# Kernel tuning notes

Hardware: AMD Instinct MI355X
Metric: run time of the kernel (lower is better)

The kernel has to match this reference:

```python
import jax, jax.numpy as jnp
import numpy as np

N = 262144          # total nodes in batched graph
B = 2048            # number of graphs
IN_DIM = 512        # in_dim == hidden_dim (required by GRUCell usage)
HID = 512
OUT_DIM = 128
TIMESTEPS = 2


def setup_inputs() -> dict:
    key = jax.random.key(0)
    ks = jax.random.split(key, 12)
    s = 0.02
    x = jax.random.normal(ks[0], (N, IN_DIM), dtype=jnp.float32)
    # sorted random segment ids: ragged graph sizes, node -> graph id
    segment_ids = jnp.sort(jax.random.randint(ks[1], (N,), 0, B, dtype=jnp.int32))
    return {
        "x": x,
        "segment_ids": segment_ids,
        "w_att_l": jax.random.normal(ks[2], (IN_DIM,), dtype=jnp.float32) * s,
        "w_att_r": jax.random.normal(ks[3], (IN_DIM,), dtype=jnp.float32) * s,
        "W_node": jax.random.normal(ks[4], (IN_DIM, HID), dtype=jnp.float32) * s,
        "W_ih": jax.random.normal(ks[5], (3 * HID, HID), dtype=jnp.float32) * s,
        "W_hh": jax.random.normal(ks[6], (3 * HID, HID), dtype=jnp.float32) * s,
        "b_ih": jax.random.normal(ks[7], (3 * HID,), dtype=jnp.float32) * s,
        "b_hh": jax.random.normal(ks[8], (3 * HID,), dtype=jnp.float32) * s,
        "W_lin": jax.random.normal(ks[9], (HID, OUT_DIM), dtype=jnp.float32) * s,
        "b_lin": jax.random.normal(ks[10], (OUT_DIM,), dtype=jnp.float32) * s,
    }


def _segment_softmax(alpha, seg, num_segments):
    # numerically stable per-graph softmax over nodes
    m = jax.ops.segment_max(alpha, seg, num_segments=num_segments)
    e = jnp.exp(alpha - m[seg])
    denom = jax.ops.segment_sum(e, seg, num_segments=num_segments)
    return e / denom[seg]


def _gru_cell(inp, h, W_ih, W_hh, b_ih, b_hh):
    gi = inp @ W_ih.T + b_ih          # [B, 3H]
    gh = h @ W_hh.T + b_hh            # [B, 3H]
    gi_r, gi_z, gi_n = jnp.split(gi, 3, axis=-1)
    gh_r, gh_z, gh_n = jnp.split(gh, 3, axis=-1)
    r = jax.nn.sigmoid(gi_r + gh_r)
    z = jax.nn.sigmoid(gi_z + gh_z)
    n = jnp.tanh(gi_n + r * gh_n)
    return (1.0 - z) * n + z * h


def reference(x, segment_ids, w_att_l, w_att_r, W_node, W_ih, W_hh, b_ih, b_hh, W_lin, b_lin):
    seg = segment_ids
    # SumPooling: per-graph sum of node features -> initial GRU hidden state
    out = jax.ops.segment_sum(x, seg, num_segments=B)      # [B, IN_DIM]
    # src_feats (x) are constant across timesteps -> precompute projections
    left_att = x @ w_att_l                                  # [N]
    h_neighbors = x @ W_node                                # [N, HID]
    for _ in range(TIMESTEPS):
        right_att = out @ w_att_r                           # [B]
        alpha = jax.nn.leaky_relu(left_att + right_att[seg], negative_slope=0.01)
        scores = _segment_softmax(alpha, seg, B)            # [N]
        msg = h_neighbors * scores[:, None]                 # [N, HID]
        gat_out = jax.ops.segment_sum(msg, seg, num_segments=B)  # [B, HID]
        h = jax.nn.elu(gat_out)
        # dropout is identity in eval mode
        out = jax.nn.silu(_gru_cell(h, out, W_ih, W_hh, b_ih, b_hh))
    return out @ W_lin + b_lin                              # [B, OUT_DIM]
```

## Files before the change

kernel.cpp:

```cpp
#include <hip/hip_runtime.h>
#include <hip/hip_bf16.h>
#include <cstdint>
#include <cstddef>

#define N_NODES 262144
#define NGRAPH  2048
#define DIM     512
#define HID3    1536
#define OUTD    128

typedef __attribute__((ext_vector_type(8))) short  short8;
typedef __attribute__((ext_vector_type(4))) float  floatx4;
typedef __attribute__((ext_vector_type(2))) float  floatx2;

__device__ inline unsigned short f2bf(float f) {
    union { float f; uint32_t u; } v; v.f = f;
    uint32_t u = v.u;
    return (unsigned short)((u + 0x7fffu + ((u >> 16) & 1u)) >> 16);
}
__device__ inline float bf2f(unsigned short h) {
    union { uint32_t u; float f; } v; v.u = ((uint32_t)h) << 16; return v.f;
}

__device__ __forceinline__ void gload_lds16(const void* g, void* l) {
    __builtin_amdgcn_global_load_lds((const __attribute__((address_space(1))) void*)g,
                                     (__attribute__((address_space(3))) void*)l, 16, 0, 0);
}

__global__ __launch_bounds__(256) void k_prep(const float* __restrict__ Wih,
        const float* __restrict__ Whh, const float* __restrict__ Wnode,
        const int* __restrict__ seg, unsigned short* __restrict__ Wihb,
        unsigned short* __restrict__ Whhb, unsigned short* __restrict__ WnT,
        int* __restrict__ starts) {
    __shared__ float tile[32][33];
    int id = blockIdx.x, t = threadIdx.x;
    if (id < 3072) {
        int i = id * 256 + t; Wihb[i] = f2bf(Wih[i]);
    } else if (id < 6144) {
        int i = (id - 3072) * 256 + t; Whhb[i] = f2bf(Whh[i]);
    } else if (id < 6400) {
        int idx = id - 6144;
        int bx = idx >> 4, by = idx & 15;
        int tx = t & 31, ty = t >> 5;
        for (int r = 0; r < 32; r += 8)
            tile[ty + r][tx] = Wnode[(size_t)(bx * 32 + ty + r) * DIM + by * 32 + tx];
        __syncthreads();
        for (int r = 0; r < 32; r += 8)
            WnT[(size_t)(by * 32 + ty + r) * DIM + bx * 32 + tx] = f2bf(tile[tx][ty + r]);
    } else {
        int b = (id - 6400) * 256 + t;
        if (b <= NGRAPH) {
            int lo = 0, hi = N_NODES;
            while (lo < hi) { int mid = (lo + hi) >> 1; if (seg[mid] < b) lo = mid + 1; else hi = mid; }
            starts[b] = lo;
        }
    }
}

template<bool WRITE_XQ>
__global__ __launch_bounds__(256) void k_init(const float* __restrict__ x,
        const int* __restrict__ starts, const float* __restrict__ watl,
        float* __restrict__ left_att, float* __restrict__ hcur,
        unsigned short* __restrict__ hcur_bf, unsigned char* __restrict__ xq) {
    __shared__ float wl[DIM];
    __shared__ float red[4 * DIM];
    int b = blockIdx.x, t = threadIdx.x;
    wl[t] = watl[t]; wl[t + 256] = watl[t + 256];
    __syncthreads();
    int s = starts[b], e = starts[b + 1];
    int w = t >> 6, lane = t & 63;
    int f0 = lane * 4;
    float acc[8] = {0.f,0.f,0.f,0.f,0.f,0.f,0.f,0.f};

    auto proc = [&](int i, floatx4 v0, floatx4 v1) {
        acc[0] += v0[0]; acc[1] += v0[1]; acc[2] += v0[2]; acc[3] += v0[3];
        acc[4] += v1[0]; acc[5] += v1[1]; acc[6] += v1[2]; acc[7] += v1[3];
        float dot = v0[0]*wl[f0] + v0[1]*wl[f0+1] + v0[2]*wl[f0+2] + v0[3]*wl[f0+3]
                  + v1[0]*wl[256+f0] + v1[1]*wl[256+f0+1] + v1[2]*wl[256+f0+2] + v1[3]*wl[256+f0+3];
        #pragma unroll
        for (int off = 32; off > 0; off >>= 1) dot += __shfl_xor(dot, off);
        if (lane == 0) left_att[i] = dot;
        if constexpr (WRITE_XQ) {
            unsigned int q0 = (unsigned int)__builtin_amdgcn_cvt_pk_fp8_f32(v0[0], v0[1], 0, false);
            q0 = (unsigned int)__builtin_amdgcn_cvt_pk_fp8_f32(v0[2], v0[3], (int)q0, true);
            unsigned int q1 = (unsigned int)__builtin_amdgcn_cvt_pk_fp8_f32(v1[0], v1[1], 0, false);
            q1 = (unsigned int)__builtin_amdgcn_cvt_pk_fp8_f32(v1[2], v1[3], (int)q1, true);
            *reinterpret_cast<unsigned int*>(xq + (size_t)i * DIM + f0) = q0;
            *reinterpret_cast<unsigned int*>(xq + (size_t)i * DIM + 256 + f0) = q1;
        }
    };

    int i = s + w;
    for (; i + 4 < e; i += 8) {
        floatx4 a0 = __builtin_nontemporal_load(reinterpret_cast<const floatx4*>(x + (size_t)i * DIM + f0));
        floatx4 a1 = __builtin_nontemporal_load(reinterpret_cast<const floatx4*>(x + (size_t)i * DIM + 256 + f0));
        floatx4 b0 = __builtin_nontemporal_load(reinterpret_cast<const floatx4*>(x + (size_t)(i + 4) * DIM + f0));
        floatx4 b1 = __builtin_nontemporal_load(reinterpret_cast<const floatx4*>(x + (size_t)(i + 4) * DIM + 256 + f0));
        proc(i, a0, a1);
        proc(i + 4, b0, b1);
    }
    if (i < e) {
        floatx4 a0 = __builtin_nontemporal_load(reinterpret_cast<const floatx4*>(x + (size_t)i * DIM + f0));
        floatx4 a1 = __builtin_nontemporal_load(reinterpret_cast<const floatx4*>(x + (size_t)i * DIM + 256 + f0));
        proc(i, a0, a1);
    }

    #pragma unroll
    for (int j = 0; j < 4; j++) {
        red[w * DIM + f0 + j]       = acc[j];
        red[w * DIM + 256 + f0 + j] = acc[4 + j];
    }
    __syncthreads();
    float s0 = red[t]       + red[DIM + t]       + red[2*DIM + t]       + red[3*DIM + t];
    float s1 = red[256 + t] + red[DIM + 256 + t] + red[2*DIM + 256 + t] + red[3*DIM + 256 + t];
    hcur[(size_t)b * DIM + t] = s0;
    hcur[(size_t)b * DIM + 256 + t] = s1;
    hcur_bf[(size_t)b * DIM + t] = f2bf(s0);
    hcur_bf[(size_t)b * DIM + 256 + t] = f2bf(s1);
}

template<bool XQ>
__global__ __launch_bounds__(256) void k_att(const float* __restrict__ x,
        const unsigned char* __restrict__ xq, const float* __restrict__ left,
        const int* __restrict__ starts, const float* __restrict__ hcur,
        const float* __restrict__ watr, unsigned short* __restrict__ swbf) {
    __shared__ float red[4 * DIM];
    __shared__ float rsh[4];
    __shared__ float rsm[4];
    __shared__ float rscal[4];
    int b = blockIdx.x, t = threadIdx.x;
    int w = t >> 6, lane = t & 63;

    float p = hcur[(size_t)b * DIM + t] * watr[t] + hcur[(size_t)b * DIM + 256 + t] * watr[256 + t];
    #pragma unroll
    for (int off = 32; off > 0; off >>= 1) p += __shfl_xor(p, off);
    if (lane == 0) rsh[w] = p;
    int s = starts[b], e = starts[b + 1];
    __syncthreads();
    float ra = rsh[0] + rsh[1] + rsh[2] + rsh[3];

    float m = -1e30f;
    for (int i = s + t; i < e; i += 256) {
        float a = left[i] + ra; a = a >= 0.f ? a : 0.01f * a;
        m = fmaxf(m, a);
    }
    #pragma unroll
    for (int off = 32; off > 0; off >>= 1) m = fmaxf(m, __shfl_xor(m, off));
    if (lane == 0) rsm[w] = m;
    __syncthreads();
    m = fmaxf(fmaxf(rsm[0], rsm[1]), fmaxf(rsm[2], rsm[3]));

    float acc[8] = {0.f,0.f,0.f,0.f,0.f,0.f,0.f,0.f};
    float esum = 0.f;
    if constexpr (XQ) {
        int f0 = lane * 8;
        auto qacc = [&](uint2 q, float ev) {
            floatx2 p0 = __builtin_amdgcn_cvt_pk_f32_fp8((int)q.x, false);
            floatx2 p1 = __builtin_amdgcn_cvt_pk_f32_fp8((int)q.x, true);
            floatx2 p2 = __builtin_amdgcn_cvt_pk_f32_fp8((int)q.y, false);
            floatx2 p3 = __builtin_amdgcn_cvt_pk_f32_fp8((int)q.y, true);
            acc[0] += ev * p0[0]; acc[1] += ev * p0[1];
            acc[2] += ev * p1[0]; acc[3] += ev * p1[1];
            acc[4] += ev * p2[0]; acc[5] += ev * p2[1];
            acc[6] += ev * p3[0]; acc[7] += ev * p3[1];
        };
        int i = s + w;
        for (; i + 4 < e; i += 8) {
            uint2 q0 = *reinterpret_cast<const uint2*>(xq + (size_t)i * DIM + f0);
            uint2 q1 = *reinterpret_cast<const uint2*>(xq + (size_t)(i + 4) * DIM + f0);
            float a0 = left[i] + ra;     a0 = a0 >= 0.f ? a0 : 0.01f * a0;
            float a1 = left[i + 4] + ra; a1 = a1 >= 0.f ? a1 : 0.01f * a1;
            float e0 = __expf(a0 - m), e1 = __expf(a1 - m);
            esum += e0 + e1;
            qacc(q0, e0);
            qacc(q1, e1);
        }
        if (i < e) {
            uint2 q0 = *reinterpret_cast<const uint2*>(xq + (size_t)i * DIM + f0);
            float a0 = left[i] + ra; a0 = a0 >= 0.f ? a0 : 0.01f * a0;
            float e0 = __expf(a0 - m);
            esum += e0;
            qacc(q0, e0);
        }
        #pragma unroll
        for (int j = 0; j < 8; j++) red[w * DIM + f0 + j] = acc[j];
    } else {
        int f0 = lane * 4;
        for (int i = s + w; i < e; i += 4) {
            float a0 = left[i] + ra; a0 = a0 >= 0.f ? a0 : 0.01f * a0;
            float e0 = __expf(a0 - m);
            esum += e0;
            float4 v0 = *reinterpret_cast<const float4*>(x + (size_t)i * DIM + f0);
            float4 v1 = *reinterpret_cast<const float4*>(x + (size_t)i * DIM + 256 + f0);
            acc[0] += e0 * v0.x; acc[1] += e0 * v0.y; acc[2] += e0 * v0.z; acc[3] += e0 * v0.w;
            acc[4] += e0 * v1.x; acc[5] += e0 * v1.y; acc[6] += e0 * v1.z; acc[7] += e0 * v1.w;
        }
        #pragma unroll
        for (int j = 0; j < 4; j++) {
            red[w * DIM + f0 + j]       = acc[j];
            red[w * DIM + 256 + f0 + j] = acc[4 + j];
        }
    }
    #pragma unroll
    for (int off = 32; off > 0; off >>= 1) esum += __shfl_xor(esum, off);
    if (lane == 0) rscal[w] = esum;
    __syncthreads();
    float tot = rscal[0] + rscal[1] + rscal[2] + rscal[3];
    float inv = tot > 0.f ? 1.0f / tot : 0.0f;
    float s0 = (red[t]       + red[DIM + t]       + red[2*DIM + t]       + red[3*DIM + t])       * inv;
    float s1 = (red[256 + t] + red[DIM + 256 + t] + red[2*DIM + 256 + t] + red[3*DIM + 256 + t]) * inv;
    swbf[(size_t)b * DIM + t] = f2bf(s0);
    swbf[(size_t)b * DIM + 256 + t] = f2bf(s1);
}

__global__ __launch_bounds__(256, 2) void k_gemm(const unsigned short* __restrict__ A0,
        const unsigned short* __restrict__ Wt0, float* __restrict__ Cf0,
        unsigned short* __restrict__ Cb0, int Ncols0, int ny0,
        const unsigned short* __restrict__ A1, const unsigned short* __restrict__ Wt1,
        float* __restrict__ Cf1, unsigned short* __restrict__ Cb1, int Ncols1) {
    const int z = blockIdx.z;
    if (z == 0 && (int)blockIdx.y >= ny0) return;
    const unsigned short* A  = z ? A1  : A0;
    const unsigned short* Wt = z ? Wt1 : Wt0;
    float* Cf          = z ? Cf1 : Cf0;
    unsigned short* Cb = z ? Cb1 : Cb0;
    const int Ncols    = z ? Ncols1 : Ncols0;

    __shared__ __align__(16) unsigned short lA[2][128 * 64];
    __shared__ __align__(16) unsigned short lW[2][128 * 64];

    int t = threadIdx.x;
    int w = t >> 6, lane = t & 63;
    int wr = w >> 1, wc = w & 1;
    int mbase = blockIdx.x * 128;
    int nbase = blockIdx.y * 128;
    int fr = lane & 15, hi = lane >> 4;
    int swz_r = (fr & 7) << 4;

    int rbase = t >> 3;
    int cole = ((((t & 7) * 16) ^ ((rbase & 7) << 4)) >> 1);
    int ldsoff = t * 16;

    floatx4 acc[4][4];
    #pragma unroll
    for (int m = 0; m < 4; m++)
        #pragma unroll
        for (int n = 0; n < 4; n++) {
            acc[m][n][0] = 0.f; acc[m][n][1] = 0.f; acc[m][n][2] = 0.f; acc[m][n][3] = 0.f;
        }

    const unsigned short* gA = A  + (size_t)(mbase + rbase) * DIM + cole;
    const unsigned short* gW = Wt + (size_t)(nbase + rbase) * DIM + cole;

    auto stage = [&](int kk, int buf) {
        #pragma unroll
        for (int c = 0; c < 4; ++c) {
            gload_lds16(gA + (size_t)(c * 32) * DIM + kk, (char*)&lA[buf][0] + c * 4096 + ldsoff);
            gload_lds16(gW + (size_t)(c * 32) * DIM + kk, (char*)&lW[buf][0] + c * 4096 + ldsoff);
        }
    };

    stage(0, 0);
    __syncthreads();
    int cur = 0;
    for (int it = 0; it < 8; ++it) {
        if (it < 7) stage((it + 1) * 64, cur ^ 1);
        #pragma unroll
        for (int ks = 0; ks < 2; ++ks) {
            short8 af[4], bf[4];
            int bc = (ks * 64 + hi * 16) ^ swz_r;
            #pragma unroll
            for (int m = 0; m < 4; ++m) {
                int row = wr * 64 + m * 16 + fr;
                af[m] = *reinterpret_cast<const short8*>(&lA[cur][(row * 128 + bc) >> 1]);
            }
            #pragma unroll
            for (int n = 0; n < 4; ++n) {
                int row = wc * 64 + n * 16 + fr;
                bf[n] = *reinterpret_cast<const short8*>(&lW[cur][(row * 128 + bc) >> 1]);
            }
            #pragma unroll
            for (int m = 0; m < 4; ++m)
                #pragma unroll
                for (int n = 0; n < 4; ++n)
                    acc[m][n] = __builtin_amdgcn_mfma_f32_16x16x32_bf16(af[m], bf[n], acc[m][n], 0, 0, 0);
        }
        if (it < 7) __syncthreads();
        cur ^= 1;
    }

    int rq = hi * 4;
    #pragma unroll
    for (int m = 0; m < 4; m++) {
        #pragma unroll
        for (int n = 0; n < 4; n++) {
            int col = nbase + wc * 64 + n * 16 + fr;
            #pragma unroll
            for (int r = 0; r < 4; r++) {
                int row = mbase + wr * 64 + m * 16 + rq + r;
                float v = acc[m][n][r];
                if (Cb) {
                    v = v > 0.f ? v : (__expf(v) - 1.0f);
                    Cb[(size_t)row * Ncols + col] = f2bf(v);
                } else {
                    Cf[(size_t)row * Ncols + col] = v;
                }
            }
        }
    }
}

__global__ __launch_bounds__(256) void k_gate(const float* __restrict__ gi,
        const float* __restrict__ gh, const float* __restrict__ bih,
        const float* __restrict__ bhh, float* __restrict__ hcur,
        unsigned short* __restrict__ hcur_bf) {
    int idx = blockIdx.x * 256 + threadIdx.x;
    int b = idx >> 7, j = (idx & 127) << 2;
    size_t gb = (size_t)b * HID3;
    floatx4 gir = *reinterpret_cast<const floatx4*>(gi + gb + j);
    floatx4 giz = *reinterpret_cast<const floatx4*>(gi + gb + 512 + j);
    floatx4 gin = *reinterpret_cast<const floatx4*>(gi + gb + 1024 + j);
    floatx4 ghr = *reinterpret_cast<const floatx4*>(gh + gb + j);
    floatx4 ghz = *reinterpret_cast<const floatx4*>(gh + gb + 512 + j);
    floatx4 ghn = *reinterpret_cast<const floatx4*>(gh + gb + 1024 + j);
    floatx4 bir = *reinterpret_cast<const floatx4*>(bih + j);
    floatx4 biz = *reinterpret_cast<const floatx4*>(bih + 512 + j);
    floatx4 bin = *reinterpret_cast<const floatx4*>(bih + 1024 + j);
    floatx4 bhr = *reinterpret_cast<const floatx4*>(bhh + j);
    floatx4 bhz = *reinterpret_cast<const floatx4*>(bhh + 512 + j);
    floatx4 bhn = *reinterpret_cast<const floatx4*>(bhh + 1024 + j);
    floatx4 hp  = *reinterpret_cast<const floatx4*>(hcur + (size_t)b * DIM + j);
    floatx4 ov;
    ushort4 ob;
    #pragma unroll
    for (int r = 0; r < 4; r++) {
        float rg = 1.0f / (1.0f + __expf(-(gir[r] + bir[r] + ghr[r] + bhr[r])));
        float zg = 1.0f / (1.0f + __expf(-(giz[r] + biz[r] + ghz[r] + bhz[r])));
        float nn = tanhf(gin[r] + bin[r] + rg * (ghn[r] + bhn[r]));
        float nh = (1.0f - zg) * nn + zg * hp[r];
        float o = nh / (1.0f + __expf(-nh));
        ov[r] = o;
        reinterpret_cast<unsigned short*>(&ob)[r] = f2bf(o);
    }
    *reinterpret_cast<floatx4*>(hcur + (size_t)b * DIM + j) = ov;
    *reinterpret_cast<ushort4*>(hcur_bf + (size_t)b * DIM + j) = ob;
}

__global__ __launch_bounds__(128) void k_fin(const float* __restrict__ hcur,
        const float* __restrict__ Wlin, const float* __restrict__ blin,
        float* __restrict__ out) {
    __shared__ float rows[16 * DIM];
    int t = threadIdx.x;
    int b0 = blockIdx.x * 16;
    for (int i = t; i < 16 * DIM / 4; i += 128)
        reinterpret_cast<float4*>(rows)[i] = reinterpret_cast<const float4*>(hcur + (size_t)b0 * DIM)[i];
    __syncthreads();
    float acc[16];
    #pragma unroll
    for (int r = 0; r < 16; r++) acc[r] = 0.f;
    #pragma unroll 4
    for (int k = 0; k < DIM; k++) {
        float wv = Wlin[k * OUTD + t];
        #pragma unroll
        for (int r = 0; r < 16; r++) acc[r] += rows[r * DIM + k] * wv;
    }
    float bl = blin[t];
    #pragma unroll
    for (int r = 0; r < 16; r++) out[(size_t)(b0 + r) * OUTD + t] = acc[r] + bl;
}

extern "C" void kernel_launch(void* const* d_in, const int* in_sizes, int n_in,
                              void* d_out, int out_size, void* d_ws, size_t ws_size,
                              hipStream_t stream) {
    const float* x     = (const float*)d_in[0];
    const int*   seg   = (const int*)d_in[1];
    const float* watl  = (const float*)d_in[2];
    const float* watr  = (const float*)d_in[3];
    const float* Wnode = (const float*)d_in[4];
    const float* Wih   = (const float*)d_in[5];
    const float* Whh   = (const float*)d_in[6];
    const float* bih   = (const float*)d_in[7];
    const float* bhh   = (const float*)d_in[8];
    const float* Wlin  = (const float*)d_in[9];
    const float* blin  = (const float*)d_in[10];
    float* out = (float*)d_out;

    char* ws = (char*)d_ws;
    size_t off = 0;
    auto alloc = [&](size_t bytes) -> void* {
        void* p = ws + off;
        off += bytes;
        off = (off + 255) & ~(size_t)255;
        return p;
    };
    float*          left    = (float*)          alloc((size_t)N_NODES * sizeof(float));
    float*          hcur    = (float*)          alloc((size_t)NGRAPH * DIM * sizeof(float));
    unsigned short* hcurbf  = (unsigned short*) alloc((size_t)NGRAPH * DIM * 2);
    unsigned short* hgbf    = (unsigned short*) alloc((size_t)NGRAPH * DIM * 2);
    unsigned short* swbf    = (unsigned short*) alloc((size_t)NGRAPH * DIM * 2);
    float*          gi      = (float*)          alloc((size_t)NGRAPH * HID3 * sizeof(float));
    float*          gh      = (float*)          alloc((size_t)NGRAPH * HID3 * sizeof(float));
    unsigned short* WnT     = (unsigned short*) alloc((size_t)DIM * DIM * 2);
    unsigned short* Wihb    = (unsigned short*) alloc((size_t)HID3 * DIM * 2);
    unsigned short* Whhb    = (unsigned short*) alloc((size_t)HID3 * DIM * 2);
    int*            starts  = (int*)            alloc((NGRAPH + 1) * sizeof(int));
    unsigned char*  xq      = (unsigned char*)(ws + off);
    bool use_xq = (off + (size_t)N_NODES * DIM) <= ws_size;

    k_prep<<<6409, 256, 0, stream>>>(Wih, Whh, Wnode, seg, Wihb, Whhb, WnT, starts);

    if (use_xq)
        k_init<true ><<<NGRAPH, 256, 0, stream>>>(x, starts, watl, left, hcur, hcurbf, xq);
    else
        k_init<false><<<NGRAPH, 256, 0, stream>>>(x, starts, watl, left, hcur, hcurbf, nullptr);

    for (int ts = 0; ts < 2; ts++) {
        if (use_xq)
            k_att<true ><<<NGRAPH, 256, 0, stream>>>(x, xq, left, starts, hcur, watr, swbf);
        else
            k_att<false><<<NGRAPH, 256, 0, stream>>>(x, xq, left, starts, hcur, watr, swbf);
        k_gemm<<<dim3(NGRAPH / 128, HID3 / 128, 2), 256, 0, stream>>>(
            swbf, WnT, nullptr, hgbf, DIM, DIM / 128,
            hcurbf, Whhb, gh, nullptr, HID3);
        k_gemm<<<dim3(NGRAPH / 128, HID3 / 128, 1), 256, 0, stream>>>(
            hgbf, Wihb, gi, nullptr, HID3, HID3 / 128,
            nullptr, nullptr, nullptr, nullptr, 0);
        k_gate<<<(NGRAPH * 128) / 256, 256, 0, stream>>>(gi, gh, bih, bhh, hcur, hcurbf);
    }
    k_fin<<<NGRAPH / 16, 128, 0, stream>>>(hcur, Wlin, blin, out);
}
```

Before: 301.4 us.

## Fuse prep into init, and GRU gate into attention and final linear kernels

Merges the weight-conversion, transpose and segment-start search into the init kernel's grid, so each graph block runs its own binary search. Drops the standalone GRU gate kernel: step 2's gate is computed at the start of the attention kernel, and the final gate inside the output linear kernel. This removes three launches and one round trip of hcur through global memory per gate. In exchange, the gate work in k_fin is done by fewer threads and blocks than the old kernel used.

```diff
diff --git a/kernel.cpp b/kernel.cpp
--- a/kernel.cpp
+++ b/kernel.cpp
@@ -27,47 +27,60 @@
                                      (__attribute__((address_space(3))) void*)l, 16, 0, 0);
 }
 
-__global__ __launch_bounds__(256) void k_prep(const float* __restrict__ Wih,
-        const float* __restrict__ Whh, const float* __restrict__ Wnode,
-        const int* __restrict__ seg, unsigned short* __restrict__ Wihb,
-        unsigned short* __restrict__ Whhb, unsigned short* __restrict__ WnT,
-        int* __restrict__ starts) {
-    __shared__ float tile[32][33];
-    int id = blockIdx.x, t = threadIdx.x;
-    if (id < 3072) {
-        int i = id * 256 + t; Wihb[i] = f2bf(Wih[i]);
-    } else if (id < 6144) {
-        int i = (id - 3072) * 256 + t; Whhb[i] = f2bf(Whh[i]);
-    } else if (id < 6400) {
-        int idx = id - 6144;
+__device__ __forceinline__ int lbound(const int* __restrict__ seg, int b) {
+    int lo = 0, hi = N_NODES;
+    while (lo < hi) { int mid = (lo + hi) >> 1; if (seg[mid] < b) lo = mid + 1; else hi = mid; }
+    return lo;
+}
+
+template<bool WRITE_XQ>
+__global__ __launch_bounds__(256) void k_init(const float* __restrict__ x,
+        const int* __restrict__ seg, const float* __restrict__ watl,
+        const float* __restrict__ Wih, const float* __restrict__ Whh,
+        const float* __restrict__ Wnode,
+        float* __restrict__ left_att, float* __restrict__ hcur,
+        unsigned short* __restrict__ hcur_bf, unsigned char* __restrict__ xq,
+        unsigned short* __restrict__ Wihb, unsigned short* __restrict__ Whhb,
+        unsigned short* __restrict__ WnT, int* __restrict__ starts) {
+    int t = threadIdx.x;
+    int bid = blockIdx.x;
+
+    if (bid >= 3584) {
+        __shared__ float tile[32][33];
+        int idx = bid - 3584;
         int bx = idx >> 4, by = idx & 15;
         int tx = t & 31, ty = t >> 5;
+        #pragma unroll
         for (int r = 0; r < 32; r += 8)
             tile[ty + r][tx] = Wnode[(size_t)(bx * 32 + ty + r) * DIM + by * 32 + tx];
         __syncthreads();
+        #pragma unroll
         for (int r = 0; r < 32; r += 8)
             WnT[(size_t)(by * 32 + ty + r) * DIM + bx * 32 + tx] = f2bf(tile[tx][ty + r]);
-    } else {
-        int b = (id - 6400) * 256 + t;
-        if (b <= NGRAPH) {
-            int lo = 0, hi = N_NODES;
-            while (lo < hi) { int mid = (lo + hi) >> 1; if (seg[mid] < b) lo = mid + 1; else hi = mid; }
-            starts[b] = lo;
-        }
-    }
-}
-
-template<bool WRITE_XQ>
-__global__ __launch_bounds__(256) void k_init(const float* __restrict__ x,
-        const int* __restrict__ starts, const float* __restrict__ watl,
-        float* __restrict__ left_att, float* __restrict__ hcur,
-        unsigned short* __restrict__ hcur_bf, unsigned char* __restrict__ xq) {
+        return;
+    }
+    if (bid >= 2048) {
+        int isW2 = bid >= 2816;
+        int i4 = (bid - (isW2 ? 2816 : 2048)) * 256 + t;
+        const float* src = isW2 ? Whh : Wih;
+        unsigned short* dst = isW2 ? Whhb : Wihb;
+        floatx4 a = *reinterpret_cast<const floatx4*>(src + (size_t)i4 * 4);
+        ushort4 o;
+        o.x = f2bf(a[0]); o.y = f2bf(a[1]); o.z = f2bf(a[2]); o.w = f2bf(a[3]);
+        *reinterpret_cast<ushort4*>(dst + (size_t)i4 * 4) = o;
+        return;
+    }
+
     __shared__ float wl[DIM];
     __shared__ float red[4 * DIM];
-    int b = blockIdx.x, t = threadIdx.x;
+    int b = bid;
     wl[t] = watl[t]; wl[t + 256] = watl[t + 256];
-    __syncthreads();
-    int s = starts[b], e = starts[b + 1];
+    int s = lbound(seg, b), e = lbound(seg, b + 1);
+    if (t == 0) {
+        starts[b] = s;
+        if (b == NGRAPH - 1) starts[NGRAPH] = e;
+    }
+    __syncthreads();
     int w = t >> 6, lane = t & 63;
     int f0 = lane * 4;
     float acc[8] = {0.f,0.f,0.f,0.f,0.f,0.f,0.f,0.f};
@@ -119,10 +132,13 @@
     hcur_bf[(size_t)b * DIM + 256 + t] = f2bf(s1);
 }
 
-template<bool XQ>
+template<bool XQ, bool FUSE_GATE>
 __global__ __launch_bounds__(256) void k_att(const float* __restrict__ x,
         const unsigned char* __restrict__ xq, const float* __restrict__ left,
-        const int* __restrict__ starts, const float* __restrict__ hcur,
+        const int* __restrict__ starts, float* __restrict__ hcur,
+        unsigned short* __restrict__ hcurbf,
+        const float* __restrict__ gi, const float* __restrict__ gh,
+        const float* __restrict__ bih, const float* __restrict__ bhh,
         const float* __restrict__ watr, unsigned short* __restrict__ swbf) {
     __shared__ float red[4 * DIM];
     __shared__ float rsh[4];
@@ -131,7 +147,33 @@
     int b = blockIdx.x, t = threadIdx.x;
     int w = t >> 6, lane = t & 63;
 
-    float p = hcur[(size_t)b * DIM + t] * watr[t] + hcur[(size_t)b * DIM + 256 + t] * watr[256 + t];
+    float p;
+    if constexpr (FUSE_GATE) {
+        size_t gb = (size_t)b * HID3;
+        float o01[2];
+        #pragma unroll
+        for (int half = 0; half < 2; ++half) {
+            int j = t + half * 256;
+            float gir = gi[gb + j]        + bih[j];
+            float giz = gi[gb + 512 + j]  + bih[512 + j];
+            float gin = gi[gb + 1024 + j] + bih[1024 + j];
+            float ghr = gh[gb + j]        + bhh[j];
+            float ghz = gh[gb + 512 + j]  + bhh[512 + j];
+            float ghn = gh[gb + 1024 + j] + bhh[1024 + j];
+            float rg = 1.0f / (1.0f + __expf(-(gir + ghr)));
+            float zg = 1.0f / (1.0f + __expf(-(giz + ghz)));
+            float nn = tanhf(gin + rg * ghn);
+            float hp = hcur[(size_t)b * DIM + j];
+            float nh = (1.0f - zg) * nn + zg * hp;
+            float o = nh / (1.0f + __expf(-nh));
+            hcur[(size_t)b * DIM + j] = o;
+            hcurbf[(size_t)b * DIM + j] = f2bf(o);
+            o01[half] = o;
+        }
+        p = o01[0] * watr[t] + o01[1] * watr[t + 256];
+    } else {
+        p = hcur[(size_t)b * DIM + t] * watr[t] + hcur[(size_t)b * DIM + 256 + t] * watr[256 + t];
+    }
     #pragma unroll
     for (int off = 32; off > 0; off >>= 1) p += __shfl_xor(p, off);
     if (lane == 0) rsh[w] = p;
@@ -310,50 +352,43 @@
     }
 }
 
-__global__ __launch_bounds__(256) void k_gate(const float* __restrict__ gi,
-        const float* __restrict__ gh, const float* __restrict__ bih,
-        const float* __restrict__ bhh, float* __restrict__ hcur,
-        unsigned short* __restrict__ hcur_bf) {
-    int idx = blockIdx.x * 256 + threadIdx.x;
-    int b = idx >> 7, j = (idx & 127) << 2;
-    size_t gb = (size_t)b * HID3;
-    floatx4 gir = *reinterpret_cast<const floatx4*>(gi + gb + j);
-    floatx4 giz = *reinterpret_cast<const floatx4*>(gi + gb + 512 + j);
-    floatx4 gin = *reinterpret_cast<const floatx4*>(gi + gb + 1024 + j);
-    floatx4 ghr = *reinterpret_cast<const floatx4*>(gh + gb + j);
-    floatx4 ghz = *reinterpret_cast<const floatx4*>(gh + gb + 512 + j);
-    floatx4 ghn = *reinterpret_cast<const floatx4*>(gh + gb + 1024 + j);
-    floatx4 bir = *reinterpret_cast<const floatx4*>(bih + j);
-    floatx4 biz = *reinterpret_cast<const floatx4*>(bih + 512 + j);
-    floatx4 bin = *reinterpret_cast<const floatx4*>(bih + 1024 + j);
-    floatx4 bhr = *reinterpret_cast<const floatx4*>(bhh + j);
-    floatx4 bhz = *reinterpret_cast<const floatx4*>(bhh + 512 + j);
-    floatx4 bhn = *reinterpret_cast<const floatx4*>(bhh + 1024 + j);
-    floatx4 hp  = *reinterpret_cast<const floatx4*>(hcur + (size_t)b * DIM + j);
-    floatx4 ov;
-    ushort4 ob;
-    #pragma unroll
-    for (int r = 0; r < 4; r++) {
-        float rg = 1.0f / (1.0f + __expf(-(gir[r] + bir[r] + ghr[r] + bhr[r])));
-        float zg = 1.0f / (1.0f + __expf(-(giz[r] + biz[r] + ghz[r] + bhz[r])));
-        float nn = tanhf(gin[r] + bin[r] + rg * (ghn[r] + bhn[r]));
-        float nh = (1.0f - zg) * nn + zg * hp[r];
-        float o = nh / (1.0f + __expf(-nh));
-        ov[r] = o;
-        reinterpret_cast<unsigned short*>(&ob)[r] = f2bf(o);
-    }
-    *reinterpret_cast<floatx4*>(hcur + (size_t)b * DIM + j) = ov;
-    *reinterpret_cast<ushort4*>(hcur_bf + (size_t)b * DIM + j) = ob;
-}
-
 __global__ __launch_bounds__(128) void k_fin(const float* __restrict__ hcur,
+        const float* __restrict__ gi, const float* __restrict__ gh,
+        const float* __restrict__ bih, const float* __restrict__ bhh,
         const float* __restrict__ Wlin, const float* __restrict__ blin,
         float* __restrict__ out) {
     __shared__ float rows[16 * DIM];
     int t = threadIdx.x;
     int b0 = blockIdx.x * 16;
-    for (int i = t; i < 16 * DIM / 4; i += 128)
-        reinterpret_cast<float4*>(rows)[i] = reinterpret_cast<const float4*>(hcur + (size_t)b0 * DIM)[i];
+    for (int k = 0; k < 16; ++k) {
+        int i4 = t + k * 128;
+        int bl = i4 >> 7;
+        int j  = (i4 & 127) << 2;
+        size_t gb = (size_t)(b0 + bl) * HID3;
+        floatx4 gir = *reinterpret_cast<const floatx4*>(gi + gb + j);
+        floatx4 giz = *reinterpret_cast<const floatx4*>(gi + gb + 512 + j);
+        floatx4 gin = *reinterpret_cast<const floatx4*>(gi + gb + 1024 + j);
+        floatx4 ghr = *reinterpret_cast<const floatx4*>(gh + gb + j);
+        floatx4 ghz = *reinterpret_cast<const floatx4*>(gh + gb + 512 + j);
+        floatx4 ghn = *reinterpret_cast<const floatx4*>(gh + gb + 1024 + j);
+        floatx4 bir = *reinterpret_cast<const floatx4*>(bih + j);
+        floatx4 biz = *reinterpret_cast<const floatx4*>(bih + 512 + j);
+        floatx4 bin = *reinterpret_cast<const floatx4*>(bih + 1024 + j);
+        floatx4 bhr = *reinterpret_cast<const floatx4*>(bhh + j);
+        floatx4 bhz = *reinterpret_cast<const floatx4*>(bhh + 512 + j);
+        floatx4 bhn = *reinterpret_cast<const floatx4*>(bhh + 1024 + j);
+        floatx4 hp  = *reinterpret_cast<const floatx4*>(hcur + (size_t)(b0 + bl) * DIM + j);
+        floatx4 ov;
+        #pragma unroll
+        for (int r = 0; r < 4; r++) {
+            float rg = 1.0f / (1.0f + __expf(-(gir[r] + bir[r] + ghr[r] + bhr[r])));
+            float zg = 1.0f / (1.0f + __expf(-(giz[r] + biz[r] + ghz[r] + bhz[r])));
+            float nn = tanhf(gin[r] + bin[r] + rg * (ghn[r] + bhn[r]));
+            float nh = (1.0f - zg) * nn + zg * hp[r];
+            ov[r] = nh / (1.0f + __expf(-nh));
+        }
+        *reinterpret_cast<floatx4*>(rows + (size_t)i4 * 4) = ov;
+    }
     __syncthreads();
     float acc[16];
     #pragma unroll
@@ -407,25 +442,35 @@
     unsigned char*  xq      = (unsigned char*)(ws + off);
     bool use_xq = (off + (size_t)N_NODES * DIM) <= ws_size;
 
-    k_prep<<<6409, 256, 0, stream>>>(Wih, Whh, Wnode, seg, Wihb, Whhb, WnT, starts);
-
     if (use_xq)
-        k_init<true ><<<NGRAPH, 256, 0, stream>>>(x, starts, watl, left, hcur, hcurbf, xq);
+        k_init<true ><<<3840, 256, 0, stream>>>(x, seg, watl, Wih, Whh, Wnode,
+                left, hcur, hcurbf, xq, Wihb, Whhb, WnT, starts);
     else
-        k_init<false><<<NGRAPH, 256, 0, stream>>>(x, starts, watl, left, hcur, hcurbf, nullptr);
+        k_init<false><<<3840, 256, 0, stream>>>(x, seg, watl, Wih, Whh, Wnode,
+                left, hcur, hcurbf, nullptr, Wihb, Whhb, WnT, starts);
 
     for (int ts = 0; ts < 2; ts++) {
-        if (use_xq)
-            k_att<true ><<<NGRAPH, 256, 0, stream>>>(x, xq, left, starts, hcur, watr, swbf);
-        else
-            k_att<false><<<NGRAPH, 256, 0, stream>>>(x, xq, left, starts, hcur, watr, swbf);
+        if (use_xq) {
+            if (ts == 0)
+                k_att<true , false><<<NGRAPH, 256, 0, stream>>>(x, xq, left, starts,
+                        hcur, hcurbf, gi, gh, bih, bhh, watr, swbf);
+            else
+                k_att<true , true ><<<NGRAPH, 256, 0, stream>>>(x, xq, left, starts,
+                        hcur, hcurbf, gi, gh, bih, bhh, watr, swbf);
+        } else {
+            if (ts == 0)
+                k_att<false, false><<<NGRAPH, 256, 0, stream>>>(x, xq, left, starts,
+                        hcur, hcurbf, gi, gh, bih, bhh, watr, swbf);
+            else
+                k_att<false, true ><<<NGRAPH, 256, 0, stream>>>(x, xq, left, starts,
+                        hcur, hcurbf, gi, gh, bih, bhh, watr, swbf);
+        }
         k_gemm<<<dim3(NGRAPH / 128, HID3 / 128, 2), 256, 0, stream>>>(
             swbf, WnT, nullptr, hgbf, DIM, DIM / 128,
             hcurbf, Whhb, gh, nullptr, HID3);
         k_gemm<<<dim3(NGRAPH / 128, HID3 / 128, 1), 256, 0, stream>>>(
             hgbf, Wihb, gi, nullptr, HID3, HID3 / 128,
             nullptr, nullptr, nullptr, nullptr, 0);
-        k_gate<<<(NGRAPH * 128) / 256, 256, 0, stream>>>(gi, gh, bih, bhh, hcur, hcurbf);
-    }
-    k_fin<<<NGRAPH / 16, 128, 0, stream>>>(hcur, Wlin, blin, out);
-}
+    }
+    k_fin<<<NGRAPH / 16, 128, 0, stream>>>(hcur, gi, gh, bih, bhh, Wlin, blin, out);
+}
```

After: 300.9 us. Within noise of the previous version (-0.2%).
